# Kernel optimization log

Hardware: AMD Instinct MI355X
Metric: run time of the kernel (lower is better)

## Reference

```python
import jax, jax.numpy as jnp
import numpy as np

B, S, D = 8, 1024, 768
H = 12            # atten_heads
DH = D // H       # head dim = 64
F = 3072          # liner_dim
EPS = 1e-6


def _layer_norm(x, gamma, beta):
    mu = jnp.mean(x, axis=-1, keepdims=True)
    var = jnp.mean(jnp.square(x - mu), axis=-1, keepdims=True)
    return (x - mu) * jax.lax.rsqrt(var + EPS) * gamma + beta


def setup_inputs() -> dict:
    key = jax.random.key(0)
    ks = jax.random.split(key, 12)
    s = 0.02
    return {
        "x": jax.random.normal(ks[0], (B, S, D), jnp.float32),
        "Wq": jax.random.normal(ks[1], (D, D), jnp.float32) * s,
        "bq": jnp.zeros((D,), jnp.float32),
        "Wk": jax.random.normal(ks[2], (D, D), jnp.float32) * s,
        "bk": jnp.zeros((D,), jnp.float32),
        "Wv": jax.random.normal(ks[3], (D, D), jnp.float32) * s,
        "bv": jnp.zeros((D,), jnp.float32),
        "Wo": jax.random.normal(ks[4], (D, D), jnp.float32) * s,
        "bo": jnp.zeros((D,), jnp.float32),
        "g1": jnp.ones((D,), jnp.float32),
        "beta1": jnp.zeros((D,), jnp.float32),
        "g2": jnp.ones((D,), jnp.float32),
        "beta2": jnp.zeros((D,), jnp.float32),
        "W1": jax.random.normal(ks[5], (D, F), jnp.float32) * s,
        "b1": jnp.zeros((F,), jnp.float32),
        "W2": jax.random.normal(ks[6], (F, D), jnp.float32) * s,
        "b2": jnp.zeros((D,), jnp.float32),
    }


def reference(x, Wq, bq, Wk, bk, Wv, bv, Wo, bo, g1, beta1, g2, beta2, W1, b1, W2, b2):
    # pre-LN
    h = _layer_norm(x, g1, beta1)                       # [B,S,D]
    # QKV projections; tf.split(axis=-1)+concat(axis=0) == per-head view
    q = (h @ Wq + bq).reshape(B, S, H, DH)
    k = (h @ Wk + bk).reshape(B, S, H, DH)
    v = (h @ Wv + bv).reshape(B, S, H, DH)
    scale = 1.0 / jnp.sqrt(jnp.float32(DH))
    scores = jnp.einsum('bqhd,bkhd->bhqk', q, k) * scale  # [B,H,S,S]
    attn = jax.nn.softmax(scores, axis=-1)
    ctx = jnp.einsum('bhqk,bkhd->bqhd', attn, v).reshape(B, S, D)
    attn_out = ctx @ Wo + bo
    x2 = attn_out + x                                    # residual (dropout=0 at eval)
    # MLP block with exact (erf) GELU, as keras.activations.gelu default
    y = _layer_norm(x2, g2, beta2)
    y = jax.nn.gelu(y @ W1 + b1, approximate=False)
    y = y @ W2 + b2
    return x2 + y
```

## Files before the change

kernel.cpp:

```cpp
#include <hip/hip_runtime.h>
#include <stdint.h>

__device__ __forceinline__ float b2f(uint16_t u) {
    union { uint32_t i; float f; } v; v.i = ((uint32_t)u) << 16; return v.f;
}
__device__ __forceinline__ float b2f_lo(uint32_t u) {
    union { uint32_t i; float f; } v; v.i = u << 16; return v.f;
}
__device__ __forceinline__ float b2f_hi(uint32_t u) {
    union { uint32_t i; float f; } v; v.i = u & 0xFFFF0000u; return v.f;
}
__device__ __forceinline__ uint16_t f2b(float f) {
    union { float f; uint32_t i; } v; v.f = f;
    uint32_t r = v.i + 0x7FFF + ((v.i >> 16) & 1);
    return (uint16_t)(r >> 16);
}

typedef short  fragAB __attribute__((ext_vector_type(8)));
typedef float  fragC  __attribute__((ext_vector_type(4)));

#define MFMA(a, b, c) __builtin_amdgcn_mfma_f32_16x16x32_bf16((a), (b), (c), 0, 0, 0)

__device__ __forceinline__ void gload_lds16(const uint16_t* g, uint16_t* l) {
    __builtin_amdgcn_global_load_lds(
        (const __attribute__((address_space(1))) void*)g,
        (__attribute__((address_space(3))) void*)l, 16, 0, 0);
}

__global__ void detect_kernel(const uint16_t* __restrict__ g1, int* __restrict__ flag) {
    if (threadIdx.x == 0 && blockIdx.x == 0)
        flag[0] = (g1[0] == 0x3F80) ? 0 : 1;
}

__global__ __launch_bounds__(256) void convert_small_kernel(
    const void* p0, const void* p1, const void* p2, const void* p3, const void* p4,
    const void* p5, const void* p6, const void* p7, const void* p8, const void* p9,
    uint16_t* __restrict__ out, const int* __restrict__ flag)
{
    const int f = *flag;
    const void* p; int n; int off;
    switch (blockIdx.x) {
        case 0: p = p0; n = 768;  off = 0;    break;
        case 1: p = p1; n = 768;  off = 768;  break;
        case 2: p = p2; n = 768;  off = 1536; break;
        case 3: p = p3; n = 768;  off = 2304; break;
        case 4: p = p4; n = 768;  off = 3072; break;
        case 5: p = p5; n = 768;  off = 3840; break;
        case 6: p = p6; n = 768;  off = 4608; break;
        case 7: p = p7; n = 768;  off = 5376; break;
        case 8: p = p8; n = 3072; off = 6144; break;
        default: p = p9; n = 768; off = 9216; break;
    }
    uint16_t* o = out + off;
    for (int i = threadIdx.x; i < n; i += 256)
        o[i] = f ? f2b(((const float*)p)[i]) : ((const uint16_t*)p)[i];
}

__global__ __launch_bounds__(256) void transpose_kernel(
    const void* __restrict__ in, uint16_t* __restrict__ out, int R, int C,
    const int* __restrict__ flag)
{
    __shared__ uint16_t tile[32][33];
    const int f  = *flag;
    const int tx = threadIdx.x & 31;
    const int ty = threadIdx.x >> 5;
    const int r0 = blockIdx.y * 32, c0 = blockIdx.x * 32;
    #pragma unroll
    for (int i = 0; i < 32; i += 8) {
        size_t idx = (size_t)(r0 + ty + i) * C + c0 + tx;
        tile[ty + i][tx] = f ? f2b(((const float*)in)[idx]) : ((const uint16_t*)in)[idx];
    }
    __syncthreads();
    #pragma unroll
    for (int i = 0; i < 32; i += 8)
        out[(size_t)(c0 + ty + i) * R + r0 + tx] = tile[tx][ty + i];
}

__global__ __launch_bounds__(256) void convert_ln_kernel(
    const void* __restrict__ xraw, const int* __restrict__ flag,
    const uint16_t* __restrict__ g, const uint16_t* __restrict__ beta,
    uint16_t* __restrict__ xb, uint16_t* __restrict__ out)
{
    const int lane = threadIdx.x & 63;
    const int wave = threadIdx.x >> 6;
    const int row  = blockIdx.x * 4 + wave;
    uint32_t* xrow = (uint32_t*)(xb + (size_t)row * 768);
    float v[12];
    if (*flag) {
        const float2* xr = (const float2*)((const float*)xraw + (size_t)row * 768);
        #pragma unroll
        for (int i = 0; i < 6; i++) {
            float2 t = xr[i * 64 + lane];
            uint16_t a = f2b(t.x), b = f2b(t.y);
            xrow[i * 64 + lane] = (uint32_t)a | ((uint32_t)b << 16);
            v[2 * i] = b2f(a); v[2 * i + 1] = b2f(b);
        }
    } else {
        const uint32_t* xr = (const uint32_t*)xraw + (size_t)row * 384;
        #pragma unroll
        for (int i = 0; i < 6; i++) {
            uint32_t u = xr[i * 64 + lane];
            xrow[i * 64 + lane] = u;
            v[2 * i] = b2f_lo(u); v[2 * i + 1] = b2f_hi(u);
        }
    }
    float sum = 0.f, sq = 0.f;
    #pragma unroll
    for (int j = 0; j < 12; j++) { sum += v[j]; sq += v[j] * v[j]; }
    #pragma unroll
    for (int off = 32; off > 0; off >>= 1) {
        sum += __shfl_xor(sum, off);
        sq  += __shfl_xor(sq, off);
    }
    const float invn = 1.0f / 768.0f;
    float mu  = sum * invn;
    float var = sq * invn - mu * mu;
    float rs  = rsqrtf(var + 1e-6f);
    uint32_t* orow = (uint32_t*)(out + (size_t)row * 768);
    const uint32_t* gp = (const uint32_t*)g;
    const uint32_t* bp = (const uint32_t*)beta;
    #pragma unroll
    for (int i = 0; i < 6; i++) {
        int p = i * 64 + lane;
        uint32_t gu = gp[p], bu = bp[p];
        float o0 = (v[2 * i]     - mu) * rs * b2f_lo(gu) + b2f_lo(bu);
        float o1 = (v[2 * i + 1] - mu) * rs * b2f_hi(gu) + b2f_hi(bu);
        orow[p] = (uint32_t)f2b(o0) | ((uint32_t)f2b(o1) << 16);
    }
}

__global__ __launch_bounds__(256) void finish_ln_kernel(
    const uint16_t* __restrict__ pa, const uint16_t* __restrict__ pb,
    const uint16_t* __restrict__ bias, const uint16_t* __restrict__ res,
    const uint16_t* __restrict__ g, const uint16_t* __restrict__ beta,
    uint16_t* __restrict__ x2, uint16_t* __restrict__ out)
{
    const int lane = threadIdx.x & 63;
    const int wave = threadIdx.x >> 6;
    const int row  = blockIdx.x * 4 + wave;
    const uint32_t* par = (const uint32_t*)pa  + (size_t)row * 384;
    const uint32_t* pbr = (const uint32_t*)pb  + (size_t)row * 384;
    const uint32_t* rr  = (const uint32_t*)res + (size_t)row * 384;
    const uint32_t* bb  = (const uint32_t*)bias;
    uint32_t* x2r = (uint32_t*)(x2 + (size_t)row * 768);
    float v[12];
    float sum = 0.f, sq = 0.f;
    #pragma unroll
    for (int i = 0; i < 6; i++) {
        int p = i * 64 + lane;
        uint32_t ua = par[p], ub = pbr[p], ur = rr[p], uc = bb[p];
        float s0 = b2f_lo(ua) + b2f_lo(ub) + b2f_lo(uc) + b2f_lo(ur);
        float s1 = b2f_hi(ua) + b2f_hi(ub) + b2f_hi(uc) + b2f_hi(ur);
        uint16_t q0 = f2b(s0), q1 = f2b(s1);
        x2r[p] = (uint32_t)q0 | ((uint32_t)q1 << 16);
        float a = b2f(q0), b = b2f(q1);
        v[2 * i] = a; v[2 * i + 1] = b;
        sum += a + b; sq += a * a + b * b;
    }
    #pragma unroll
    for (int off = 32; off > 0; off >>= 1) {
        sum += __shfl_xor(sum, off);
        sq  += __shfl_xor(sq, off);
    }
    const float invn = 1.0f / 768.0f;
    float mu  = sum * invn;
    float var = sq * invn - mu * mu;
    float rs  = rsqrtf(var + 1e-6f);
    uint32_t* orow = (uint32_t*)(out + (size_t)row * 768);
    const uint32_t* gp = (const uint32_t*)g;
    const uint32_t* bp = (const uint32_t*)beta;
    #pragma unroll
    for (int i = 0; i < 6; i++) {
        int p = i * 64 + lane;
        uint32_t gu = gp[p], bu = bp[p];
        float o0 = (v[2 * i]     - mu) * rs * b2f_lo(gu) + b2f_lo(bu);
        float o1 = (v[2 * i + 1] - mu) * rs * b2f_hi(gu) + b2f_hi(bu);
        orow[p] = (uint32_t)f2b(o0) | ((uint32_t)f2b(o1) << 16);
    }
}

__global__ __launch_bounds__(256) void gemm_kernel(
    const uint16_t* __restrict__ A, const uint16_t* __restrict__ Wt,
    const uint16_t* __restrict__ bias, uint16_t* __restrict__ out,
    uint16_t* __restrict__ outB, int M, int N, int K, int mode)
{
    __shared__ __align__(16) uint16_t As[128 * 32];
    __shared__ __align__(16) uint16_t Bs[128 * 32];
    __shared__ __align__(16) uint16_t Es[4 * 1152];
    const int tid  = threadIdx.x;
    const int lane = tid & 63;
    const int wave = tid >> 6;
    const int wm   = (wave >> 1) * 64;
    const int wn   = (wave & 1) * 64;
    const int qrow = lane & 15;
    const int quad = lane >> 4;

    const int gx = gridDim.x, gy = gridDim.y, gz = gridDim.z;
    const int flat = blockIdx.x + gx * (blockIdx.y + gy * blockIdx.z);
    const int xcd = flat & 7;
    const int local = flat >> 3;
    const int n0 = (local % gx) * 128;
    const int mz = (local / gx) * 8 + xcd;
    const int m0 = (mz % gy) * 128;
    const int slice = mz / gy;
    const int kLen = K / gz;
    const int kOff = slice * kLen;

    const int srow = lane >> 2;
    const int pcol = lane & 3;
    const int g = (pcol - (srow >> 1)) & 3;
    const uint16_t* aG0 = A  + (size_t)(m0 + wave * 16 + srow) * K + kOff + g * 8;
    const uint16_t* aG1 = A  + (size_t)(m0 + (4 + wave) * 16 + srow) * K + kOff + g * 8;
    const uint16_t* bG0 = Wt + (size_t)(n0 + wave * 16 + srow) * K + kOff + g * 8;
    const uint16_t* bG1 = Wt + (size_t)(n0 + (4 + wave) * 16 + srow) * K + kOff + g * 8;
    uint16_t* asD0 = &As[wave * 512];
    uint16_t* asD1 = &As[(4 + wave) * 512];
    uint16_t* bsD0 = &Bs[wave * 512];
    uint16_t* bsD1 = &Bs[(4 + wave) * 512];

    const int pchunk = (quad + (qrow >> 1)) & 3;
    const uint16_t* arB = &As[(wm + qrow) * 32 + pchunk * 8];
    const uint16_t* brB = &Bs[(wn + qrow) * 32 + pchunk * 8];

    fragC acc[4][4] = {};

    for (int k0 = 0; k0 < kLen; k0 += 32) {
        __syncthreads();
        gload_lds16(aG0 + k0, asD0);
        gload_lds16(aG1 + k0, asD1);
        gload_lds16(bG0 + k0, bsD0);
        gload_lds16(bG1 + k0, bsD1);
        __syncthreads();
        fragAB af[4], bf[4];
        #pragma unroll
        for (int t = 0; t < 4; t++) {
            af[t] = *(const fragAB*)(arB + t * 512);
            bf[t] = *(const fragAB*)(brB + t * 512);
        }
        #pragma unroll
        for (int mi = 0; mi < 4; mi++)
            #pragma unroll
            for (int ni = 0; ni < 4; ni++)
                acc[mi][ni] = MFMA(af[mi], bf[ni], acc[mi][ni]);
    }

    uint16_t* po = (mode == 7 && slice) ? outB : out;
    uint16_t* eb = &Es[wave * 1152];
    float bvv[4];
    if (mode != 7) {
        #pragma unroll
        for (int ni = 0; ni < 4; ni++) bvv[ni] = b2f(bias[n0 + wn + ni * 16 + qrow]);
    }
    const int er = lane >> 2, ec = (lane & 3) * 16;
    #pragma unroll
    for (int mi = 0; mi < 4; mi++) {
        #pragma unroll
        for (int ni = 0; ni < 4; ni++) {
            #pragma unroll
            for (int r = 0; r < 4; r++) {
                float v = acc[mi][ni][r];
                if (mode != 7) {
                    v += bvv[ni];
                    if (mode == 2) {
                        float arg = v * (1.5957691216f + 0.0713548163f * v * v);
                        v = v * __builtin_amdgcn_rcpf(1.0f + __expf(-arg));
                    }
                }
                eb[(quad * 4 + r) * 72 + ni * 16 + qrow] = f2b(v);
            }
        }
        __asm__ volatile("s_waitcnt lgkmcnt(0)" ::: "memory");
        uint16_t* dst = po + (size_t)(m0 + wm + mi * 16 + er) * N + n0 + wn + ec;
        *(int4*)dst       = *(const int4*)&eb[er * 72 + ec];
        *(int4*)(dst + 8) = *(const int4*)&eb[er * 72 + ec + 8];
        __asm__ volatile("" ::: "memory");
    }
}

__global__ __launch_bounds__(256) void finish_kernel(
    const uint16_t* __restrict__ pa, const uint16_t* __restrict__ pb,
    const uint16_t* __restrict__ bias, const uint16_t* __restrict__ res,
    void* __restrict__ out, const int* __restrict__ flag)
{
    const int i = (blockIdx.x * 256 + threadIdx.x) * 4;
    const int n = i % 768;
    ushort4 av = *(const ushort4*)(pa + i);
    ushort4 pv = *(const ushort4*)(pb + i);
    ushort4 rv = *(const ushort4*)(res + i);
    ushort4 cv = *(const ushort4*)(bias + n);
    float o0 = b2f(av.x) + b2f(pv.x) + b2f(cv.x) + b2f(rv.x);
    float o1 = b2f(av.y) + b2f(pv.y) + b2f(cv.y) + b2f(rv.y);
    float o2 = b2f(av.z) + b2f(pv.z) + b2f(cv.z) + b2f(rv.z);
    float o3 = b2f(av.w) + b2f(pv.w) + b2f(cv.w) + b2f(rv.w);
    if (flag && *flag) {
        *(float4*)((float*)out + i) = make_float4(o0, o1, o2, o3);
    } else {
        ushort4 ov;
        ov.x = f2b(o0); ov.y = f2b(o1); ov.z = f2b(o2); ov.w = f2b(o3);
        *(ushort4*)((uint16_t*)out + i) = ov;
    }
}

__global__ __launch_bounds__(256) void attn_kernel(
    const uint16_t* __restrict__ QKV, uint16_t* __restrict__ ctx)
{
    __shared__ __align__(16) uint16_t Ks[128 * 72];
    __shared__ __align__(16) uint16_t Vs[64 * 72];
    __shared__ __align__(16) uint16_t Ps[4][2][16 * 72];
    const int tid  = threadIdx.x;
    const int lane = tid & 63;
    const int wave = tid >> 6;
    const int qrow = lane & 15;
    const int quad = lane >> 4;

    const int flat = blockIdx.x + 8 * blockIdx.y;
    const int xcd = flat & 7, local = flat >> 3;
    const int bh = xcd * 12 + (local >> 3);
    const int b  = bh / 12, hh = bh % 12;
    const int q0blk = (local & 7) * 128;
    const int q0 = q0blk + wave * 32;

    const uint16_t* base = QKV + (size_t)b * 1024 * 2304;
    const uint16_t* Qp = base + hh * 64;
    const uint16_t* Kp = base + 768 + hh * 64;
    const uint16_t* Vp = base + 1536 + hh * 64;

    const int srow = tid >> 2;
    const int scol = (tid & 3) * 16;
    const int pkey = srow ^ scol;

    fragAB qf[2][2];
    #pragma unroll
    for (int qq = 0; qq < 2; qq++)
        #pragma unroll
        for (int c = 0; c < 2; c++)
            qf[qq][c] = *(const fragAB*)(Qp + (size_t)(q0 + qq * 16 + qrow) * 2304 + c * 32 + quad * 8);

    fragC ao[2][4] = {};
    float lsum[2][4] = {};

    for (int kk = 0; kk < 1024; kk += 64) {
        __syncthreads();
        *(int4*)&Ks[srow * 72 + scol]     = *(const int4*)(Kp + (size_t)(kk + srow) * 2304 + scol);
        *(int4*)&Ks[srow * 72 + scol + 8] = *(const int4*)(Kp + (size_t)(kk + srow) * 2304 + scol + 8);
        {
            union { int4 q[2]; uint16_t u[16]; } t;
            t.q[0] = *(const int4*)(Vp + (size_t)(kk + srow) * 2304 + scol);
            t.q[1] = *(const int4*)(Vp + (size_t)(kk + srow) * 2304 + scol + 8);
            #pragma unroll
            for (int j = 0; j < 16; j++)
                Vs[(scol + j) * 72 + pkey] = t.u[j];
        }
        __syncthreads();

        fragC sc[2][4] = {};
        #pragma unroll
        for (int g = 0; g < 4; g++) {
            fragAB kf0 = *(const fragAB*)&Ks[(g * 16 + qrow) * 72 + quad * 8];
            fragAB kf1 = *(const fragAB*)&Ks[(g * 16 + qrow) * 72 + 32 + quad * 8];
            #pragma unroll
            for (int qq = 0; qq < 2; qq++) {
                sc[qq][g] = MFMA(qf[qq][0], kf0, sc[qq][g]);
                sc[qq][g] = MFMA(qf[qq][1], kf1, sc[qq][g]);
            }
        }

        #pragma unroll
        for (int qq = 0; qq < 2; qq++)
            #pragma unroll
            for (int g = 0; g < 4; g++)
                #pragma unroll
                for (int r = 0; r < 4; r++) {
                    float p = __expf(fminf(sc[qq][g][r] * 0.125f, 20.0f));
                    lsum[qq][r] += p;
                    Ps[wave][qq][(quad * 4 + r) * 72 + g * 16 + qrow] = f2b(p);
                }
        __syncthreads();

        fragAB pf[2][2];
        #pragma unroll
        for (int qq = 0; qq < 2; qq++)
            #pragma unroll
            for (int c = 0; c < 2; c++)
                pf[qq][c] = *(const fragAB*)&Ps[wave][qq][qrow * 72 + c * 32 + quad * 8];

        #pragma unroll
        for (int f = 0; f < 4; f++) {
            fragAB vf0 = *(const fragAB*)&Vs[(f * 16 + qrow) * 72 + ((0 + quad * 8) ^ (f * 16))];
            fragAB vf1 = *(const fragAB*)&Vs[(f * 16 + qrow) * 72 + ((32 + quad * 8) ^ (f * 16))];
            #pragma unroll
            for (int qq = 0; qq < 2; qq++) {
                ao[qq][f] = MFMA(pf[qq][0], vf0, ao[qq][f]);
                ao[qq][f] = MFMA(pf[qq][1], vf1, ao[qq][f]);
            }
        }
    }

    float inv[2][4];
    #pragma unroll
    for (int qq = 0; qq < 2; qq++)
        #pragma unroll
        for (int r = 0; r < 4; r++) {
            float s = lsum[qq][r];
            #pragma unroll
            for (int off = 1; off < 16; off <<= 1) s += __shfl_xor(s, off);
            inv[qq][r] = 1.0f / s;
        }

    #pragma unroll
    for (int qq = 0; qq < 2; qq++)
        #pragma unroll
        for (int f = 0; f < 4; f++)
            #pragma unroll
            for (int r = 0; r < 4; r++)
                Ks[(wave * 32 + qq * 16 + quad * 4 + r) * 72 + f * 16 + qrow] =
                    f2b(ao[qq][f][r] * inv[qq][r]);
    __syncthreads();
    {
        const int row = tid >> 1, half = tid & 1;
        uint16_t* dst = ctx + (size_t)(b * 1024 + q0blk + row) * 768 + hh * 64 + half * 32;
        const uint16_t* src = &Ks[row * 72 + half * 32];
        *(int4*)dst        = *(const int4*)src;
        *(int4*)(dst + 8)  = *(const int4*)(src + 8);
        *(int4*)(dst + 16) = *(const int4*)(src + 16);
        *(int4*)(dst + 24) = *(const int4*)(src + 24);
    }
}

extern "C" void kernel_launch(void* const* d_in, const int* in_sizes, int n_in,
                              void* d_out, int out_size, void* d_ws, size_t ws_size,
                              hipStream_t stream)
{
    (void)in_sizes; (void)n_in; (void)out_size; (void)ws_size;
    const void* x_raw  = d_in[0];
    const void* Wq_raw = d_in[1];
    const void* bq_raw = d_in[2];
    const void* Wk_raw = d_in[3];
    const void* bk_raw = d_in[4];
    const void* Wv_raw = d_in[5];
    const void* bv_raw = d_in[6];
    const void* Wo_raw = d_in[7];
    const void* bo_raw = d_in[8];
    const void* g1_raw = d_in[9];
    const void* be1_raw= d_in[10];
    const void* g2_raw = d_in[11];
    const void* be2_raw= d_in[12];
    const void* W1_raw = d_in[13];
    const void* b1_raw = d_in[14];
    const void* W2_raw = d_in[15];
    const void* b2_raw = d_in[16];

    uint8_t* ws = (uint8_t*)d_ws;
    const size_t SZ = (size_t)8192 * 768 * 2;
    uint16_t* xb    = (uint16_t*)(ws);
    uint16_t* h1    = (uint16_t*)(ws + SZ);
    uint16_t* QKVb  = (uint16_t*)(ws + 2 * SZ);
    uint16_t* ctx   = (uint16_t*)(ws + 5 * SZ);
    uint16_t* pWa   = (uint16_t*)(ws + 2 * SZ);
    uint16_t* pWb   = (uint16_t*)(ws + SZ);
    uint16_t* x2    = (uint16_t*)(ws + 5 * SZ);
    uint16_t* ln2   = (uint16_t*)(ws + 6 * SZ);
    uint16_t* y1    = (uint16_t*)(ws);
    uint16_t* pMa   = (uint16_t*)(ws + 4 * SZ);
    uint16_t* pMb   = (uint16_t*)(ws + 6 * SZ);
    uint8_t*  wts   = ws + 7 * SZ;
    uint16_t* WqkvT = (uint16_t*)(wts);
    uint16_t* WoT   = (uint16_t*)(wts + 3 * 1179648);
    uint16_t* W1T   = (uint16_t*)(wts + 4 * 1179648);
    uint16_t* W2T   = (uint16_t*)(wts + 4 * 1179648 + 4718592);
    uint16_t* smallv = (uint16_t*)(wts + 4 * 1179648 + 2 * 4718592);
    int* flag = (int*)(wts + 4 * 1179648 + 2 * 4718592 + 9984 * 2);
    uint16_t* G1   = smallv + 0,    *BE1 = smallv + 768;
    uint16_t* G2   = smallv + 1536, *BE2 = smallv + 2304;
    uint16_t* BQKV = smallv + 3072;
    uint16_t* BO   = smallv + 5376;
    uint16_t* B1   = smallv + 6144, *B2 = smallv + 9216;

    dim3 blk(256);
    detect_kernel<<<1, 64, 0, stream>>>((const uint16_t*)g1_raw, flag);
    convert_small_kernel<<<10, blk, 0, stream>>>(g1_raw, be1_raw, g2_raw, be2_raw,
        bq_raw, bk_raw, bv_raw, bo_raw, b1_raw, b2_raw, smallv, flag);

    transpose_kernel<<<dim3(24, 24), blk, 0, stream>>>(Wq_raw, WqkvT,              768, 768, flag);
    transpose_kernel<<<dim3(24, 24), blk, 0, stream>>>(Wk_raw, WqkvT + 589824,     768, 768, flag);
    transpose_kernel<<<dim3(24, 24), blk, 0, stream>>>(Wv_raw, WqkvT + 2 * 589824, 768, 768, flag);
    transpose_kernel<<<dim3(24, 24), blk, 0, stream>>>(Wo_raw, WoT, 768, 768, flag);
    transpose_kernel<<<dim3(96, 24), blk, 0, stream>>>(W1_raw, W1T, 768, 3072, flag);
    transpose_kernel<<<dim3(24, 96), blk, 0, stream>>>(W2_raw, W2T, 3072, 768, flag);

    convert_ln_kernel<<<2048, blk, 0, stream>>>(x_raw, flag, G1, BE1, xb, h1);

    gemm_kernel<<<dim3(18, 64), blk, 0, stream>>>(h1, WqkvT, BQKV, QKVb, nullptr,
                                                  8192, 2304, 768, 0);

    attn_kernel<<<dim3(8, 96), blk, 0, stream>>>(QKVb, ctx);

    gemm_kernel<<<dim3(6, 64, 2), blk, 0, stream>>>(ctx, WoT, BO, pWa, pWb,
                                                    8192, 768, 768, 7);
    finish_ln_kernel<<<2048, blk, 0, stream>>>(pWa, pWb, BO, xb, G2, BE2, x2, ln2);

    gemm_kernel<<<dim3(24, 64), blk, 0, stream>>>(ln2, W1T, B1, y1, nullptr,
                                                  8192, 3072, 768, 2);

    gemm_kernel<<<dim3(6, 64, 2), blk, 0, stream>>>(y1, W2T, B2, pMa, pMb,
                                                    8192, 768, 3072, 7);
    finish_kernel<<<6144, blk, 0, stream>>>(pMa, pMb, B2, x2, d_out, flag);
}
```

Before: 324.8 us.

## Multi-stage LDS pipeline with register double-buffering in GEMM kernel

Replaces the single-buffered load/sync/compute loop of the bf16 GEMM with a 4-slot LDS ring that keeps up to three K-tiles of global-to-LDS loads in flight. LDS fragments are double-buffered in registers (even/odd), and explicit vmcnt/lgkmcnt waits plus sched_barrier and setprio order the loads around the MFMA blocks. The aim is to hide global memory latency and drop one barrier per tile. In exchange, LDS use grows to 64 KB per block, which can lower occupancy, and the loop assumes an even tile count.

```diff
diff --git a/kernel.cpp b/kernel.cpp
--- a/kernel.cpp
+++ b/kernel.cpp
@@ -184,9 +184,10 @@
     const uint16_t* __restrict__ bias, uint16_t* __restrict__ out,
     uint16_t* __restrict__ outB, int M, int N, int K, int mode)
 {
-    __shared__ __align__(16) uint16_t As[128 * 32];
-    __shared__ __align__(16) uint16_t Bs[128 * 32];
-    __shared__ __align__(16) uint16_t Es[4 * 1152];
+    __shared__ __align__(16) uint16_t lds[32768];
+    uint16_t* ldsA = lds;
+    uint16_t* ldsB = lds + 16384;
+
     const int tid  = threadIdx.x;
     const int lane = tid & 63;
     const int wave = tid >> 6;
@@ -205,6 +206,7 @@
     const int slice = mz / gy;
     const int kLen = K / gz;
     const int kOff = slice * kLen;
+    const int nt   = kLen >> 5;
 
     const int srow = lane >> 2;
     const int pcol = lane & 3;
@@ -213,39 +215,78 @@
     const uint16_t* aG1 = A  + (size_t)(m0 + (4 + wave) * 16 + srow) * K + kOff + g * 8;
     const uint16_t* bG0 = Wt + (size_t)(n0 + wave * 16 + srow) * K + kOff + g * 8;
     const uint16_t* bG1 = Wt + (size_t)(n0 + (4 + wave) * 16 + srow) * K + kOff + g * 8;
-    uint16_t* asD0 = &As[wave * 512];
-    uint16_t* asD1 = &As[(4 + wave) * 512];
-    uint16_t* bsD0 = &Bs[wave * 512];
-    uint16_t* bsD1 = &Bs[(4 + wave) * 512];
 
     const int pchunk = (quad + (qrow >> 1)) & 3;
-    const uint16_t* arB = &As[(wm + qrow) * 32 + pchunk * 8];
-    const uint16_t* brB = &Bs[(wn + qrow) * 32 + pchunk * 8];
+    const int arOff = (wm + qrow) * 32 + pchunk * 8;
+    const int brOff = (wn + qrow) * 32 + pchunk * 8;
 
     fragC acc[4][4] = {};
-
-    for (int k0 = 0; k0 < kLen; k0 += 32) {
-        __syncthreads();
-        gload_lds16(aG0 + k0, asD0);
-        gload_lds16(aG1 + k0, asD1);
-        gload_lds16(bG0 + k0, bsD0);
-        gload_lds16(bG1 + k0, bsD1);
-        __syncthreads();
-        fragAB af[4], bf[4];
-        #pragma unroll
-        for (int t = 0; t < 4; t++) {
-            af[t] = *(const fragAB*)(arB + t * 512);
-            bf[t] = *(const fragAB*)(brB + t * 512);
-        }
+    fragAB afE[4], bfE[4], afO[4], bfO[4];
+
+    auto stageT = [&](int kt) {
+        const int so = (kt & 3) * 4096;
+        const int k0 = kt * 32;
+        gload_lds16(aG0 + k0, ldsA + so + wave * 512);
+        gload_lds16(aG1 + k0, ldsA + so + (4 + wave) * 512);
+        gload_lds16(bG0 + k0, ldsB + so + wave * 512);
+        gload_lds16(bG1 + k0, ldsB + so + (4 + wave) * 512);
+    };
+    auto readF = [&](int kt, fragAB af[4], fragAB bf[4]) {
+        const uint16_t* ar = ldsA + (kt & 3) * 4096 + arOff;
+        const uint16_t* br = ldsB + (kt & 3) * 4096 + brOff;
+        #pragma unroll
+        for (int i = 0; i < 4; i++) {
+            af[i] = *(const fragAB*)(ar + i * 512);
+            bf[i] = *(const fragAB*)(br + i * 512);
+        }
+    };
+
+    stageT(0); stageT(1); stageT(2);
+    __asm__ volatile("s_waitcnt vmcnt(4)" ::: "memory");
+    __builtin_amdgcn_s_barrier();
+    readF(0, afE, bfE);
+    __asm__ volatile("s_waitcnt lgkmcnt(0)" ::: "memory");
+    __builtin_amdgcn_sched_barrier(0);
+
+    for (int t = 0; t < nt; t += 2) {
+        readF(t + 1, afO, bfO);
+        if (t + 3 < nt) stageT(t + 3);
+        __builtin_amdgcn_sched_barrier(0);
+        __builtin_amdgcn_s_setprio(1);
         #pragma unroll
         for (int mi = 0; mi < 4; mi++)
             #pragma unroll
             for (int ni = 0; ni < 4; ni++)
-                acc[mi][ni] = MFMA(af[mi], bf[ni], acc[mi][ni]);
-    }
+                acc[mi][ni] = MFMA(afE[mi], bfE[ni], acc[mi][ni]);
+        __builtin_amdgcn_s_setprio(0);
+        __asm__ volatile("s_waitcnt lgkmcnt(0)" ::: "memory");
+        __builtin_amdgcn_sched_barrier(0);
+        if (t + 3 < nt) { __asm__ volatile("s_waitcnt vmcnt(4)" ::: "memory"); }
+        else            { __asm__ volatile("s_waitcnt vmcnt(0)" ::: "memory"); }
+        __builtin_amdgcn_sched_barrier(0);
+        __builtin_amdgcn_s_barrier();
+        if (t + 2 < nt) readF(t + 2, afE, bfE);
+        if (t + 4 < nt) stageT(t + 4);
+        __builtin_amdgcn_sched_barrier(0);
+        __builtin_amdgcn_s_setprio(1);
+        #pragma unroll
+        for (int mi = 0; mi < 4; mi++)
+            #pragma unroll
+            for (int ni = 0; ni < 4; ni++)
+                acc[mi][ni] = MFMA(afO[mi], bfO[ni], acc[mi][ni]);
+        __builtin_amdgcn_s_setprio(0);
+        __asm__ volatile("s_waitcnt lgkmcnt(0)" ::: "memory");
+        __builtin_amdgcn_sched_barrier(0);
+        if (t + 4 < nt) { __asm__ volatile("s_waitcnt vmcnt(4)" ::: "memory"); }
+        else            { __asm__ volatile("s_waitcnt vmcnt(0)" ::: "memory"); }
+        __builtin_amdgcn_sched_barrier(0);
+        __builtin_amdgcn_s_barrier();
+    }
+
+    __syncthreads();
 
     uint16_t* po = (mode == 7 && slice) ? outB : out;
-    uint16_t* eb = &Es[wave * 1152];
+    uint16_t* eb = lds + wave * 1152;
     float bvv[4];
     if (mode != 7) {
         #pragma unroll
```

Measured after the change: 311.0 us. -4.2%, faster.

## Load GEMM B fragments directly from global into registers with double buffering

Applied to the files above, without the earlier changes.

The GEMM kernel no longer stages the weight tile through LDS. Each wave reads its B MFMA fragments straight from global memory into registers, using even/odd register buffers so the next k-step's fragments are prefetched while the current MFMAs run. This halves LDS traffic and shared memory use, and may raise occupancy. In exchange, B is loaded redundantly by the two waves that share columns, the global reads are less coalesced, register pressure rises, and the loop assumes an even number of k tiles.

```diff
diff --git a/kernel.cpp b/kernel.cpp
--- a/kernel.cpp
+++ b/kernel.cpp
@@ -185,7 +185,6 @@
     uint16_t* __restrict__ outB, int M, int N, int K, int mode)
 {
     __shared__ __align__(16) uint16_t As[128 * 32];
-    __shared__ __align__(16) uint16_t Bs[128 * 32];
     __shared__ __align__(16) uint16_t Es[4 * 1152];
     const int tid  = threadIdx.x;
     const int lane = tid & 63;
@@ -205,43 +204,66 @@
     const int slice = mz / gy;
     const int kLen = K / gz;
     const int kOff = slice * kLen;
+    const int nt   = kLen >> 5;
 
     const int srow = lane >> 2;
     const int pcol = lane & 3;
     const int g = (pcol - (srow >> 1)) & 3;
-    const uint16_t* aG0 = A  + (size_t)(m0 + wave * 16 + srow) * K + kOff + g * 8;
-    const uint16_t* aG1 = A  + (size_t)(m0 + (4 + wave) * 16 + srow) * K + kOff + g * 8;
-    const uint16_t* bG0 = Wt + (size_t)(n0 + wave * 16 + srow) * K + kOff + g * 8;
-    const uint16_t* bG1 = Wt + (size_t)(n0 + (4 + wave) * 16 + srow) * K + kOff + g * 8;
+    const uint16_t* aG0 = A + (size_t)(m0 + wave * 16 + srow) * K + kOff + g * 8;
+    const uint16_t* aG1 = A + (size_t)(m0 + (4 + wave) * 16 + srow) * K + kOff + g * 8;
     uint16_t* asD0 = &As[wave * 512];
     uint16_t* asD1 = &As[(4 + wave) * 512];
-    uint16_t* bsD0 = &Bs[wave * 512];
-    uint16_t* bsD1 = &Bs[(4 + wave) * 512];
 
     const int pchunk = (quad + (qrow >> 1)) & 3;
     const uint16_t* arB = &As[(wm + qrow) * 32 + pchunk * 8];
-    const uint16_t* brB = &Bs[(wn + qrow) * 32 + pchunk * 8];
+
+    const uint16_t* bB = Wt + (size_t)(n0 + wn + qrow) * K + kOff + quad * 8;
+    const size_t bStride = (size_t)16 * K;
 
     fragC acc[4][4] = {};
-
-    for (int k0 = 0; k0 < kLen; k0 += 32) {
-        __syncthreads();
-        gload_lds16(aG0 + k0, asD0);
-        gload_lds16(aG1 + k0, asD1);
-        gload_lds16(bG0 + k0, bsD0);
-        gload_lds16(bG1 + k0, bsD1);
-        __syncthreads();
-        fragAB af[4], bf[4];
-        #pragma unroll
-        for (int t = 0; t < 4; t++) {
-            af[t] = *(const fragAB*)(arB + t * 512);
-            bf[t] = *(const fragAB*)(brB + t * 512);
-        }
-        #pragma unroll
-        for (int mi = 0; mi < 4; mi++)
+    fragAB bfE[4], bfO[4];
+
+    #pragma unroll
+    for (int ni = 0; ni < 4; ni++)
+        bfE[ni] = *(const fragAB*)(bB + (size_t)ni * bStride);
+
+    for (int t = 0; t < nt; t += 2) {
+        __syncthreads();
+        gload_lds16(aG0 + t * 32, asD0);
+        gload_lds16(aG1 + t * 32, asD1);
+        #pragma unroll
+        for (int ni = 0; ni < 4; ni++)
+            bfO[ni] = *(const fragAB*)(bB + (size_t)ni * bStride + (t + 1) * 32);
+        __syncthreads();
+        {
+            fragAB af[4];
+            #pragma unroll
+            for (int i = 0; i < 4; i++) af[i] = *(const fragAB*)(arB + i * 512);
+            #pragma unroll
+            for (int mi = 0; mi < 4; mi++)
+                #pragma unroll
+                for (int ni = 0; ni < 4; ni++)
+                    acc[mi][ni] = MFMA(af[mi], bfE[ni], acc[mi][ni]);
+        }
+        __syncthreads();
+        gload_lds16(aG0 + (t + 1) * 32, asD0);
+        gload_lds16(aG1 + (t + 1) * 32, asD1);
+        if (t + 2 < nt) {
             #pragma unroll
             for (int ni = 0; ni < 4; ni++)
-                acc[mi][ni] = MFMA(af[mi], bf[ni], acc[mi][ni]);
+                bfE[ni] = *(const fragAB*)(bB + (size_t)ni * bStride + (t + 2) * 32);
+        }
+        __syncthreads();
+        {
+            fragAB af[4];
+            #pragma unroll
+            for (int i = 0; i < 4; i++) af[i] = *(const fragAB*)(arB + i * 512);
+            #pragma unroll
+            for (int mi = 0; mi < 4; mi++)
+                #pragma unroll
+                for (int ni = 0; ni < 4; ni++)
+                    acc[mi][ni] = MFMA(af[mi], bfO[ni], acc[mi][ni]);
+        }
     }
 
     uint16_t* po = (mode == 7 && slice) ? outB : out;
```

New measurement: 449.7 us. +38.4%, slower.
